# Optimization experiments

Hardware: AMD Instinct MI355X
Metric: run time of the kernel (lower is better)

Reference implementation:

```python
import jax, jax.numpy as jnp
import numpy as np

B, N, NB, E, H, A, K, D = 32, 512, 10, 1024, 256, 82, 4, 3


def setup_inputs() -> dict:
    key = jax.random.key(0)
    ks = iter(jax.random.split(key, 64))
    f = lambda shape: jax.random.normal(next(ks), shape, jnp.float32) * 0.05
    inp = {
        "atom_fea": jax.random.normal(next(ks), (B, N, A), jnp.float32),
        "bond_fea": jax.random.normal(next(ks), (B, E, 6), jnp.float32),
        "d_anb": jax.random.randint(next(ks), (B, N, NB), 0, N),
        "d_bnb": jax.random.randint(next(ks), (B, N, NB), 0, E),
        "d_nbs_mask": (jax.random.uniform(next(ks), (B, N, NB)) < 0.8).astype(jnp.float32),
        "d_mask": (jax.random.uniform(next(ks), (B, N)) < 0.9).astype(jnp.float32),
        "Wv": f((A, H)), "bv": f((H,)),
        "Wa_main": f((D, K, H, H)), "ba_main": f((D, K, H)),
        "Wa_super": f((D, K, H, H)), "ba_super": f((D, K, H)),
        "Wm": f((D, K, H, H)), "bm": f((D, K, H)),
        "Wbmm": f((D, K, H)), "bbmm": f((D, K)),
        "Wm2s": f((D, K * H, H)), "bm2s": f((D, H)),
        "Ws2m": f((D, H, H)), "bs2m": f((D, H)),
        "Wsup": f((D, H, H)), "bsup": f((D, H)),
        "Wzm1": f((D, H, H)), "bzm1": f((D, H)),
        "Wzm2": f((D, H, H)), "bzm2": f((D, H)),
        "Wzs1": f((D, H, H)), "bzs1": f((D, H)),
        "Wzs2": f((D, H, H)), "bzs2": f((D, H)),
        "Wu2": f((D, H + 6, H)), "bu2": f((D, H)),
        "Wu1": f((D, 2 * H, H)), "bu1": f((D, H)),
    }
    return inp


def mask_softmax(a, mask):
    a_max = jnp.max(a, -1, keepdims=True)
    e = jnp.exp(a - a_max) * mask
    return e / (jnp.sum(e, -1, keepdims=True) + 1e-6)


def _forward(atom_fea, bond_fea, d_nbs_mask, d_mask,
             Wv, bv, Wa_main, ba_main, Wa_super, ba_super, Wm, bm, Wbmm, bbmm,
             Wm2s, bm2s, Ws2m, bs2m, Wsup, bsup,
             Wzm1, bzm1, Wzm2, bzm2, Wzs1, bzs1, Wzs2, bzs2,
             Wu2, bu2, Wu1, bu1, d_anb, d_bnb):
    Bn = atom_fea.shape[0]
    bidx = jnp.arange(Bn)[:, None, None]
    # vertex embedding (default leaky_relu slope 0.01)
    vf = jax.nn.leaky_relu(atom_fea @ Wv + bv, 0.01)            # [B,N,H]
    sf = jnp.sum(vf * d_mask[:, :, None], axis=1, keepdims=True)  # [B,1,H]
    mask3 = d_nbs_mask[..., None]                               # [B,N,NB,1]
    for d in range(D):
        # --- multi-head main->super attention (vectorized over heads k) ---
        a_main = jnp.tanh(jnp.einsum('bnh,khj->bknj', vf, Wa_main[d]) + ba_main[d][None, :, None, :])
        a_super = jnp.tanh(jnp.einsum('boh,khj->bkoj', sf, Wa_super[d]) + ba_super[d][None, :, None, :])
        a = jnp.einsum('bknh,kh->bkn', a_main * a_super, Wbmm[d]) + bbmm[d][None, :, None]
        attn = mask_softmax(a, d_mask[:, None, :])               # [B,K,N]
        mvf = jnp.einsum('bnh,khj->bknj', vf, Wm[d]) + bm[d][None, :, None, :]
        m2s = jnp.einsum('bkn,bknh->bkh', attn, mvf).reshape(Bn, 1, K * H)
        main_to_super = jnp.tanh(m2s @ Wm2s[d] + bm2s[d])        # [B,1,H]
        # --- wln unit: gather neighbors, MLP, masked sum (slope 0.1) ---
        vnei = vf[bidx, d_anb]                                   # [B,N,NB,H]
        enei = bond_fea[bidx, d_bnb]                             # [B,N,NB,6]
        lnei = jnp.concatenate([vnei, enei], -1)                 # [B,N,NB,H+6]
        nei = jax.nn.leaky_relu(lnei @ Wu2[d] + bu2[d], 0.1)
        nei = jnp.sum(nei * mask3, axis=2)                       # [B,N,H]
        main_self = jax.nn.leaky_relu(jnp.concatenate([vf, nei], -1) @ Wu1[d] + bu1[d], 0.1)
        # --- GRU-style gated updates ---
        super_to_main = jnp.tanh(sf @ Ws2m[d] + bs2m[d])         # [B,1,H]
        super_self = jnp.tanh(sf @ Wsup[d] + bsup[d])            # [B,1,H]
        z_main = jax.nn.sigmoid(main_self @ Wzm1[d] + bzm1[d] + super_to_main @ Wzm2[d] + bzm2[d])
        vf = (1 - z_main) * main_self + z_main * super_to_main
        z_sup = jax.nn.sigmoid(super_self @ Wzs1[d] + bzs1[d] + main_to_super @ Wzs2[d] + bzs2[d])
        sf = (1 - z_sup) * super_self + z_sup * main_to_super    # [B,1,H]; sum over dim 1 is a no-op
    return vf, sf


def reference(atom_fea, bond_fea, d_anb, d_bnb, d_nbs_mask, d_mask,
              Wv, bv, Wa_main, ba_main, Wa_super, ba_super, Wm, bm, Wbmm, bbmm,
              Wm2s, bm2s, Ws2m, bs2m, Wsup, bsup,
              Wzm1, bzm1, Wzm2, bzm2, Wzs1, bzs1, Wzs2, bzs2,
              Wu2, bu2, Wu1, bu1):
    return _forward(atom_fea, bond_fea, d_nbs_mask, d_mask,
                    Wv, bv, Wa_main, ba_main, Wa_super, ba_super, Wm, bm, Wbmm, bbmm,
                    Wm2s, bm2s, Ws2m, bs2m, Wsup, bsup,
                    Wzm1, bzm1, Wzm2, bzm2, Wzs1, bzs1, Wzs2, bzs2,
                    Wu2, bu2, Wu1, bu1, d_anb, d_bnb)
```

## Files before the change

kernel.cpp:

```cpp
#include <hip/hip_runtime.h>
#include <hip/hip_bf16.h>

#define B_ 32
#define N_ 512
#define NB_ 10
#define E_ 1024
#define H_ 256
#define A_ 82
#define K_ 4
#define D_ 3
#define M_ (B_*N_)

typedef unsigned short u16;
typedef __attribute__((ext_vector_type(8))) short bf16x8;
typedef __attribute__((ext_vector_type(4))) float f32x4;

__device__ __forceinline__ float b2f(u16 u){
    unsigned int x = ((unsigned int)u) << 16;
    return __builtin_bit_cast(float, x);
}
__device__ __forceinline__ u16 f2b(float f){
    unsigned int x = __builtin_bit_cast(unsigned int, f);
    unsigned int lsb = (x >> 16) & 1u;
    x += 0x7fffu + lsb;
    return (u16)(x >> 16);
}
__device__ __forceinline__ float sigmoidf_(float x){ return 1.f/(1.f+expf(-x)); }

static constexpr int CVT_N[31] = {
    B_*E_*6, B_*N_*NB_, B_*N_,
    A_*H_, H_,
    D_*K_*H_*H_, D_*K_*H_, D_*K_*H_*H_, D_*K_*H_,
    D_*K_*H_*H_, D_*K_*H_, D_*K_*H_, D_*K_,
    D_*K_*H_*H_, D_*H_, D_*H_*H_, D_*H_,
    D_*H_*H_, D_*H_, D_*H_*H_, D_*H_,
    D_*H_*H_, D_*H_, D_*H_*H_, D_*H_,
    D_*H_*H_, D_*H_, D_*(H_+6)*H_, D_*H_,
    D_*2*H_*H_, D_*H_
};
struct Offs { long v[32]; };
static constexpr Offs mk_offs(){
    Offs o{}; o.v[0]=0;
    for(int i=0;i<31;i++) o.v[i+1]=o.v[i]+CVT_N[i];
    return o;
}
static constexpr Offs CVT_OFF = mk_offs();

struct Ptrs { const void* p[31]; };

__global__ void k_detect(const unsigned short* __restrict__ wv_raw, int* __restrict__ flag){
    float v = b2f(wv_raw[threadIdx.x]);
    bool plaus = (v==v) && (fabsf(v) < 100.0f);
    unsigned long long m = __ballot(plaus);
    if (threadIdx.x==0) *flag = (m == ~0ULL) ? 1 : 0;
}

__global__ void k_cvt(Ptrs ptrs, float* __restrict__ dst, const int* __restrict__ flag){
    int t = blockIdx.y;
    int n = CVT_N[t];
    int i4 = blockIdx.x*256 + threadIdx.x;
    if (i4*4 >= n) return;
    const void* src = ptrs.p[t];
    float4 o;
    if (*flag){
        ushort4 u = ((const ushort4*)src)[i4];
        o.x=b2f(u.x); o.y=b2f(u.y); o.z=b2f(u.z); o.w=b2f(u.w);
    } else {
        o = ((const float4*)src)[i4];
    }
    *(float4*)(dst + CVT_OFF.v[t] + (size_t)i4*4) = o;
}

__global__ void k_wt(const float* __restrict__ Wam, const float* __restrict__ Wu2,
                     const float* __restrict__ Wu1, const float* __restrict__ Wzm1,
                     u16* __restrict__ WT){
    int mi = blockIdx.z;
    const float* src;
    if (mi<12)      src = Wam  + (size_t)mi*H_*H_;
    else if (mi<15) src = Wu2  + (size_t)(mi-12)*(H_+6)*H_;
    else if (mi<18) src = Wu1  + (size_t)(mi-15)*2*H_*H_;
    else if (mi<21) src = Wu1  + (size_t)(mi-18)*2*H_*H_ + (size_t)H_*H_;
    else            src = Wzm1 + (size_t)(mi-21)*H_*H_;
    __shared__ float t[32][33];
    int x = threadIdx.x, y = threadIdx.y;
    int k0 = blockIdx.y*32, n0 = blockIdx.x*32;
    for(int yy=y; yy<32; yy+=8) t[yy][x] = src[(size_t)(k0+yy)*H_ + n0+x];
    __syncthreads();
    u16* dst = WT + ((size_t)mi*8 + (k0>>5))*8192;
    int quad = x>>3, j = x&7;
    for(int yy=y; yy<32; yy+=8){
        int n = n0+yy, nt = n>>4, lv = n&15;
        dst[nt*512 + quad*128 + lv*8 + j] = f2b(t[x][yy]);
    }
}

__global__ void k_embed(const u16* __restrict__ atom, const float* __restrict__ Wv,
                        const float* __restrict__ bv, float* __restrict__ vf,
                        u16* __restrict__ vf_bf, const int* __restrict__ flag){
    __shared__ float arow[8][A_];
    int r0 = blockIdx.x*8; int j = threadIdx.x;
    int fl = *flag;
    for(int i=j;i<8*A_;i+=256){
        int r=i/A_, a=i-r*A_;
        arow[r][a] = fl ? b2f(atom[(size_t)(r0+r)*A_+a])
                        : ((const float*)atom)[(size_t)(r0+r)*A_+a];
    }
    __syncthreads();
    float acc[8];
    float bj = bv[j];
    #pragma unroll
    for(int r=0;r<8;r++) acc[r]=bj;
    for(int a=0;a<A_;a++){
        float w = Wv[a*H_+j];
        #pragma unroll
        for(int r=0;r<8;r++) acc[r] += arow[r][a]*w;
    }
    #pragma unroll
    for(int r=0;r<8;r++){
        float v = acc[r];
        v = v>0.f ? v : 0.01f*v;
        vf[(size_t)(r0+r)*H_+j] = v;
        vf_bf[(size_t)(r0+r)*H_+j] = f2b(v);
    }
}

__global__ void k_sf0(const float* __restrict__ vf, const float* __restrict__ dmask,
                      float* __restrict__ sf){
    int b = blockIdx.x, h = threadIdx.x;
    __shared__ float mk[N_];
    for(int n=threadIdx.x;n<N_;n+=256) mk[n] = dmask[b*N_+n];
    __syncthreads();
    float s=0.f;
    #pragma unroll 8
    for(int n=0;n<N_;n++) s += mk[n]*vf[((size_t)b*N_+n)*H_ + h];
    sf[b*H_+h]=s;
}

__global__ void k_s1(int d, const float* __restrict__ sf,
    const float* __restrict__ Was, const float* __restrict__ bas,
    const float* __restrict__ Wbmm,
    const float* __restrict__ Ws2m, const float* __restrict__ bs2m,
    const float* __restrict__ Wsup, const float* __restrict__ bsup,
    float* __restrict__ asw, float* __restrict__ s2m, float* __restrict__ ssf)
{
    int b = blockIdx.x, m = blockIdx.y, j = threadIdx.x;
    __shared__ float sfl[H_];
    sfl[j] = sf[b*H_+j];
    __syncthreads();
    const float* W; float bias;
    if (m < 4){ W = Was + (size_t)(d*K_+m)*H_*H_; bias = bas[(d*K_+m)*H_+j]; }
    else if (m==4){ W = Ws2m + (size_t)d*H_*H_; bias = bs2m[d*H_+j]; }
    else { W = Wsup + (size_t)d*H_*H_; bias = bsup[d*H_+j]; }
    float acc = bias;
    #pragma unroll 8
    for(int h=0;h<H_;h++) acc += sfl[h]*W[h*H_+j];
    float v = tanhf(acc);
    if (m < 4) asw[(b*K_+m)*H_+j] = v * Wbmm[(d*K_+m)*H_+j];
    else if (m==4) s2m[b*H_+j] = v;
    else ssf[b*H_+j] = v;
}

__global__ void k_s2(int d, const float* __restrict__ s2m,
    const float* __restrict__ Wzm2, const float* __restrict__ bzm2,
    float* __restrict__ stm2p)
{
    int b=blockIdx.x, c=blockIdx.y, j=threadIdx.x;
    __shared__ float xl[64];
    if (j<64) xl[j] = s2m[b*H_ + c*64 + j];
    __syncthreads();
    const float* W = Wzm2 + (size_t)d*H_*H_ + (size_t)(c*64)*H_;
    float acc = (c==0) ? bzm2[d*H_+j] : 0.f;
    #pragma unroll 8
    for(int h=0;h<64;h++) acc += xl[h]*W[h*H_+j];
    stm2p[((size_t)c*B_+b)*H_+j] = acc;
}

__device__ __forceinline__ void stageW(const u16* __restrict__ g, u16* l){
    int t = threadIdx.x;
    const u16* gs = g + t*8;
    u16* ls = l + t*8;
    #pragma unroll
    for(int it=0; it<4; ++it)
        __builtin_amdgcn_global_load_lds(
            (const __attribute__((address_space(1))) void*)(gs + it*2048),
            (__attribute__((address_space(3))) void*)(ls + it*2048),
            16, 0, 0);
}

__device__ __forceinline__ void gemm_ldsW(const u16* __restrict__ Abf,
                                          const u16* __restrict__ WTg,
                                          u16* Wlds, f32x4 acc[2][8])
{
    int tid = threadIdx.x;
    int lane = tid & 63, wave = tid >> 6;
    int wy = wave >> 1, wx = wave & 1;
    int quad = lane >> 4, l15 = lane & 15;
    const u16* aP0 = Abf + (size_t)(wy*32 + l15)*H_ + quad*8;
    const u16* aP1 = aP0 + 16*H_;
    bf16x8 a[4][2];
    #pragma unroll
    for(int s=0;s<3;s++){
        a[s][0] = *(const bf16x8*)(aP0 + s*32);
        a[s][1] = *(const bf16x8*)(aP1 + s*32);
    }
    stageW(WTg, Wlds);
    #pragma unroll
    for(int mt=0;mt<2;mt++)
        #pragma unroll
        for(int nt=0;nt<8;nt++) acc[mt][nt]=(f32x4){0.f,0.f,0.f,0.f};
    __syncthreads();
    #pragma unroll
    for(int s=0;s<8;s++){
        if (s<7) stageW(WTg + (size_t)(s+1)*8192, Wlds + ((s+1)&1)*8192);
        if (s<5){
            int sl = s+3;
            a[sl&3][0] = *(const bf16x8*)(aP0 + sl*32);
            a[sl&3][1] = *(const bf16x8*)(aP1 + sl*32);
        }
        const u16* wb = Wlds + (s&1)*8192 + wx*4096 + quad*128 + l15*8;
        bf16x8 w[8];
        #pragma unroll
        for(int nt=0;nt<8;nt++) w[nt] = *(const bf16x8*)(wb + nt*512);
        #pragma unroll
        for(int mt=0;mt<2;mt++)
            #pragma unroll
            for(int nt=0;nt<8;nt++)
                acc[mt][nt] = __builtin_amdgcn_mfma_f32_16x16x32_bf16(
                    a[s&3][mt], w[nt], acc[mt][nt], 0,0,0);
        __syncthreads();
    }
}

__global__ __launch_bounds__(256,3) void k_gemm_big(int d, const u16* __restrict__ vf_bf,
    const u16* __restrict__ WT, const float* __restrict__ ba_main,
    const float* __restrict__ bbmm, const float* __restrict__ bu1,
    const float* __restrict__ asw, float* __restrict__ score,
    float* __restrict__ proj_u2, float* __restrict__ pu1a)
{
    __shared__ __attribute__((aligned(16))) u16 Wlds[2*8192];
    int m0 = blockIdx.x*64;
    int seg = blockIdx.y;
    int b = m0 >> 9;
    int mi;
    if (seg < 4)      mi = d*4+seg;
    else if (seg==4)  mi = 12+d;
    else              mi = 15+d;
    f32x4 acc[2][8];
    gemm_ldsW(vf_bf + (size_t)m0*H_, WT + (size_t)mi*H_*H_, Wlds, acc);
    int tid=threadIdx.x, lane=tid&63, wave=tid>>6;
    int wy=wave>>1, wx=wave&1, quad=lane>>4, l15=lane&15;
    if (seg < 4){
        float* sred = (float*)Wlds;
        const float* aswp = asw + (size_t)(b*K_+seg)*H_;
        const float* bap  = ba_main + (size_t)(d*K_+seg)*H_;
        float bbv[8], awv[8];
        #pragma unroll
        for(int nt=0;nt<8;nt++){
            int col = wx*128+nt*16+l15;
            bbv[nt]=bap[col]; awv[nt]=aswp[col];
        }
        #pragma unroll
        for(int mt=0;mt<2;mt++)
            #pragma unroll
            for(int r=0;r<4;r++){
                float p=0.f;
                #pragma unroll
                for(int nt=0;nt<8;nt++)
                    p += tanhf(acc[mt][nt][r]+bbv[nt])*awv[nt];
                int row = wy*32+mt*16+quad*4+r;
                sred[row*33 + wx*16+l15] = p;
            }
        __syncthreads();
        if (tid < 64){
            float s=0.f;
            #pragma unroll 8
            for(int i=0;i<32;i++) s += sred[tid*33+i];
            score[(size_t)(b*K_+seg)*N_ + (m0&511) + tid] = s + bbmm[d*K_+seg];
        }
    } else if (seg==4){
        #pragma unroll
        for(int mt=0;mt<2;mt++)
            #pragma unroll
            for(int nt=0;nt<8;nt++){
                int col = wx*128+nt*16+l15;
                #pragma unroll
                for(int r=0;r<4;r++){
                    int row = m0 + wy*32+mt*16+quad*4+r;
                    proj_u2[(size_t)row*H_+col] = acc[mt][nt][r];
                }
            }
    } else {
        const float* bp = bu1 + d*H_;
        #pragma unroll
        for(int mt=0;mt<2;mt++)
            #pragma unroll
            for(int nt=0;nt<8;nt++){
                int col = wx*128+nt*16+l15;
                float bb = bp[col];
                #pragma unroll
                for(int r=0;r<4;r++){
                    int row = m0 + wy*32+mt*16+quad*4+r;
                    pu1a[(size_t)row*H_+col] = acc[mt][nt][r] + bb;
                }
            }
    }
}

__global__ __launch_bounds__(256,3) void k_mainself(int d, u16* __restrict__ neims,
    const u16* __restrict__ WT, float* __restrict__ pu)
{
    __shared__ __attribute__((aligned(16))) u16 Wlds[2*8192];
    int m0 = blockIdx.x*64;
    f32x4 acc[2][8];
    gemm_ldsW(neims + (size_t)m0*H_, WT + (size_t)(18+d)*H_*H_, Wlds, acc);
    int tid=threadIdx.x, lane=tid&63, wave=tid>>6;
    int wy=wave>>1, wx=wave&1, quad=lane>>4, l15=lane&15;
    #pragma unroll
    for(int mt=0;mt<2;mt++)
        #pragma unroll
        for(int nt=0;nt<8;nt++){
            int col = wx*128+nt*16+l15;
            #pragma unroll
            for(int r=0;r<4;r++){
                int row = m0 + wy*32+mt*16+quad*4+r;
                float v = acc[mt][nt][r] + pu[(size_t)row*H_+col];
                v = v>0.f? v : 0.1f*v;
                pu[(size_t)row*H_+col] = v;
                neims[(size_t)row*H_+col] = f2b(v);
            }
        }
}

__global__ __launch_bounds__(256,3) void k_update(int d, const float* __restrict__ ms,
    const u16* __restrict__ ms_bf, const u16* __restrict__ WT, const float* __restrict__ bzm1,
    const float* __restrict__ stm2p, const float* __restrict__ s2m,
    float* __restrict__ vf, u16* __restrict__ vf_bf)
{
    __shared__ __attribute__((aligned(16))) u16 Wlds[2*8192];
    int m0 = blockIdx.x*64; int b = m0>>9;
    f32x4 acc[2][8];
    gemm_ldsW(ms_bf + (size_t)m0*H_, WT + (size_t)(21+d)*H_*H_, Wlds, acc);
    int tid=threadIdx.x, lane=tid&63, wave=tid>>6;
    int wy=wave>>1, wx=wave&1, quad=lane>>4, l15=lane&15;
    #pragma unroll
    for(int mt=0;mt<2;mt++)
        #pragma unroll
        for(int nt=0;nt<8;nt++){
            int col = wx*128+nt*16+l15;
            float bz = bzm1[d*H_+col];
            float st = stm2p[(size_t)(0*B_+b)*H_+col] + stm2p[(size_t)(1*B_+b)*H_+col]
                     + stm2p[(size_t)(2*B_+b)*H_+col] + stm2p[(size_t)(3*B_+b)*H_+col];
            float sm = s2m[b*H_+col];
            #pragma unroll
            for(int r=0;r<4;r++){
                int row = m0 + wy*32+mt*16+quad*4+r;
                float z = sigmoidf_(acc[mt][nt][r] + bz + st);
                float msv = ms[(size_t)row*H_+col];
                float o = (1.f-z)*msv + z*sm;
                vf[(size_t)row*H_+col] = o;
                vf_bf[(size_t)row*H_+col] = f2b(o);
            }
        }
}

__global__ void k_softmax(float* __restrict__ score, const float* __restrict__ dmask,
                          float* __restrict__ sumattn){
    int b = blockIdx.x, k = blockIdx.y;
    int tid = threadIdx.x;
    __shared__ float sh[256];
    float* a = score + (size_t)(b*K_+k)*N_;
    float v0 = a[tid], v1 = a[tid+256];
    sh[tid]=fmaxf(v0,v1); __syncthreads();
    for(int s=128;s>0;s>>=1){ if(tid<s) sh[tid]=fmaxf(sh[tid],sh[tid+s]); __syncthreads(); }
    float m = sh[0]; __syncthreads();
    float e0 = expf(v0-m)*dmask[b*N_+tid], e1 = expf(v1-m)*dmask[b*N_+tid+256];
    sh[tid]=e0+e1; __syncthreads();
    for(int s=128;s>0;s>>=1){ if(tid<s) sh[tid]+=sh[tid+s]; __syncthreads(); }
    float S = sh[0];
    float inv = 1.f/(S+1e-6f);
    a[tid]=e0*inv; a[tid+256]=e1*inv;
    if(tid==0) sumattn[b*K_+k]=S*inv;
}

__global__ void k_t2(const float* __restrict__ attn, const float* __restrict__ vf,
                     float* __restrict__ tpart){
    int b=blockIdx.x, k=blockIdx.y, c=blockIdx.z, h=threadIdx.x;
    __shared__ float at[256];
    at[h] = attn[(size_t)(b*K_+k)*N_ + c*256 + h];
    __syncthreads();
    float acc=0.f;
    const float* vfp = vf + ((size_t)b*N_ + c*256)*H_ + h;
    #pragma unroll 8
    for(int n=0;n<256;n++) acc += at[n]*vfp[(size_t)n*H_];
    tpart[((size_t)(c*B_+b)*K_+k)*H_+h]=acc;
}

__global__ void k_m1(int d, const float* __restrict__ tpart, const float* __restrict__ sumattn,
    const float* __restrict__ Wm, const float* __restrict__ bm, float* __restrict__ m2s)
{
    int b=blockIdx.x, k=blockIdx.y, j=threadIdx.x;
    __shared__ float tl[H_];
    tl[j] = tpart[((size_t)(0*B_+b)*K_+k)*H_+j] + tpart[((size_t)(1*B_+b)*K_+k)*H_+j];
    __syncthreads();
    const float* W = Wm + (size_t)(d*K_+k)*H_*H_;
    float acc = sumattn[b*K_+k]*bm[(d*K_+k)*H_+j];
    #pragma unroll 8
    for(int h=0;h<H_;h++) acc += tl[h]*W[h*H_+j];
    m2s[(size_t)(b*K_+k)*H_+j]=acc;
}

__global__ void k_m2(int d, const float* __restrict__ m2s, const float* __restrict__ Wm2s,
                     float* __restrict__ mtsp)
{
    int b=blockIdx.x, c=blockIdx.y, j=threadIdx.x;
    __shared__ float xl[H_];
    xl[j]=m2s[(size_t)(b*K_+c)*H_+j];
    __syncthreads();
    const float* W = Wm2s + (size_t)d*(K_*H_)*H_ + (size_t)(c*H_)*H_;
    float acc=0.f;
    #pragma unroll 8
    for(int h=0;h<H_;h++) acc += xl[h]*W[h*H_+j];
    mtsp[((size_t)c*B_+b)*H_+j]=acc;
}

__global__ void k_mts(int d, const float* __restrict__ mtsp, const float* __restrict__ bm2s,
                      float* __restrict__ mts){
    int b=blockIdx.x, j=threadIdx.x;
    float acc = bm2s[d*H_+j];
    #pragma unroll
    for(int c=0;c<4;c++) acc += mtsp[((size_t)c*B_+b)*H_+j];
    mts[b*H_+j]=tanhf(acc);
}

__global__ void k_m3(int d, const float* __restrict__ ssf, const float* __restrict__ mts,
    const float* __restrict__ Wzs1, const float* __restrict__ Wzs2,
    float* __restrict__ p1, float* __restrict__ p2)
{
    int b=blockIdx.x, m=blockIdx.y, j=threadIdx.x;
    __shared__ float xl[H_];
    const float* x = m ? mts : ssf;
    xl[j]=x[b*H_+j];
    __syncthreads();
    const float* W = (m ? Wzs2 : Wzs1) + (size_t)d*H_*H_;
    float acc=0.f;
    #pragma unroll 8
    for(int h=0;h<H_;h++) acc += xl[h]*W[h*H_+j];
    (m ? p2 : p1)[b*H_+j]=acc;
}

__global__ void k_sfup(int d, const float* __restrict__ p1, const float* __restrict__ p2,
    const float* __restrict__ bzs1, const float* __restrict__ bzs2,
    const float* __restrict__ ssf, const float* __restrict__ mts, float* __restrict__ sf)
{
    int b=blockIdx.x, j=threadIdx.x;
    float z = sigmoidf_(p1[b*H_+j]+bzs1[d*H_+j]+p2[b*H_+j]+bzs2[d*H_+j]);
    sf[b*H_+j]=(1.f-z)*ssf[b*H_+j]+z*mts[b*H_+j];
}

__global__ void k_nei(int d, const int* __restrict__ anb, const int* __restrict__ bnb,
    const float* __restrict__ nbm, const float* __restrict__ bond,
    const float* __restrict__ Wu2, const float* __restrict__ bu2,
    const float* __restrict__ proj_u2, u16* __restrict__ nei_bf)
{
    __shared__ float W2s[6][256];
    __shared__ float bfeat[4][NB_][6];
    __shared__ int ai[4][NB_]; __shared__ int bi[4][NB_]; __shared__ float mk[4][NB_];
    int r0 = blockIdx.x*4; int b = r0 >> 9; int h = threadIdx.x;
    const float* W2 = Wu2 + (size_t)d*(H_+6)*H_ + (size_t)H_*H_;
    for(int i=h;i<6*H_;i+=256) W2s[i>>8][i&255] = W2[i];
    if (h < 4*NB_){
        int r=h/NB_, jn=h-r*NB_;
        ai[r][jn]=anb[(size_t)(r0+r)*NB_+jn];
        bi[r][jn]=bnb[(size_t)(r0+r)*NB_+jn];
        mk[r][jn]=nbm[(size_t)(r0+r)*NB_+jn];
    }
    __syncthreads();
    if (h < 4*NB_*6){
        int r=h/(NB_*6), rem=h-r*(NB_*6), jn=rem/6, i=rem-jn*6;
        bfeat[r][jn][i]=bond[((size_t)b*E_+bi[r][jn])*6+i];
    }
    __syncthreads();
    float bu = bu2[d*H_+h];
    #pragma unroll
    for(int r=0;r<4;r++){
        float acc=0.f;
        #pragma unroll
        for(int jn=0;jn<NB_;jn++){
            float v = proj_u2[((size_t)b*N_+ai[r][jn])*H_+h] + bu;
            #pragma unroll
            for(int i=0;i<6;i++) v += bfeat[r][jn][i]*W2s[i][h];
            v = v>0.f? v : 0.1f*v;
            acc += mk[r][jn]*v;
        }
        nei_bf[(size_t)(r0+r)*H_+h]=f2b(acc);
    }
}

__global__ void k_out(const float* __restrict__ vf, const float* __restrict__ sf,
                      void* __restrict__ out, const int* __restrict__ flag){
    int idx = blockIdx.x*256 + threadIdx.x;
    const int total = M_*H_ + B_*H_;
    if (idx >= total) return;
    float v = (idx < M_*H_) ? vf[idx] : sf[idx - M_*H_];
    if (*flag) ((unsigned short*)out)[idx] = f2b(v);
    else       ((float*)out)[idx] = v;
}

extern "C" void kernel_launch(void* const* d_in, const int* in_sizes, int n_in,
                              void* d_out, int out_size, void* d_ws, size_t ws_size,
                              hipStream_t stream)
{
    const int* anb = (const int*)d_in[2];
    const int* bnb = (const int*)d_in[3];

    float* ws   = (float*)d_ws;
    int*   flag = (int*)ws;
    float* cvt  = ws + 64;
    float* p    = cvt + ((CVT_OFF.v[31] + 63) & ~63L);
    float* vf        = p; p += (size_t)M_*H_;
    float* proj_u2   = p; p += (size_t)M_*H_;
    float* proj_u1a  = p; p += (size_t)M_*H_;
    u16*   vf_bf     = (u16*)p; p += (size_t)M_*H_/2;
    u16*   neims     = (u16*)p; p += (size_t)M_*H_/2;
    float* sf        = p; p += B_*H_;
    float* score     = p; p += B_*K_*N_;
    float* sumattn   = p; p += B_*K_;
    float* asw       = p; p += B_*K_*H_;
    float* s2m       = p; p += B_*H_;
    float* ssf       = p; p += B_*H_;
    float* stm2p     = p; p += 4*B_*H_;
    float* tpart     = p; p += 2*B_*K_*H_;
    float* m2s       = p; p += B_*K_*H_;
    float* mtsp      = p; p += 4*B_*H_;
    float* mts       = p; p += B_*H_;
    float* p1        = p; p += B_*H_;
    float* p2        = p; p += B_*H_;
    u16*   WT        = (u16*)p;

    const float* cBond = cvt + CVT_OFF.v[0];
    const float* cNbm  = cvt + CVT_OFF.v[1];
    const float* cDm   = cvt + CVT_OFF.v[2];
    const float* cWv   = cvt + CVT_OFF.v[3];
    const float* cbv   = cvt + CVT_OFF.v[4];
    const float* cWam  = cvt + CVT_OFF.v[5];
    const float* cbam  = cvt + CVT_OFF.v[6];
    const float* cWas  = cvt + CVT_OFF.v[7];
    const float* cbas  = cvt + CVT_OFF.v[8];
    const float* cWm   = cvt + CVT_OFF.v[9];
    const float* cbm   = cvt + CVT_OFF.v[10];
    const float* cWbmm = cvt + CVT_OFF.v[11];
    const float* cbbmm = cvt + CVT_OFF.v[12];
    const float* cWm2s = cvt + CVT_OFF.v[13];
    const float* cbm2s = cvt + CVT_OFF.v[14];
    const float* cWs2m = cvt + CVT_OFF.v[15];
    const float* cbs2m = cvt + CVT_OFF.v[16];
    const float* cWsup = cvt + CVT_OFF.v[17];
    const float* cbsup = cvt + CVT_OFF.v[18];
    const float* cWzm1 = cvt + CVT_OFF.v[19];
    const float* cbzm1 = cvt + CVT_OFF.v[20];
    const float* cWzm2 = cvt + CVT_OFF.v[21];
    const float* cbzm2 = cvt + CVT_OFF.v[22];
    const float* cWzs1 = cvt + CVT_OFF.v[23];
    const float* cbzs1 = cvt + CVT_OFF.v[24];
    const float* cWzs2 = cvt + CVT_OFF.v[25];
    const float* cbzs2 = cvt + CVT_OFF.v[26];
    const float* cWu2  = cvt + CVT_OFF.v[27];
    const float* cbu2  = cvt + CVT_OFF.v[28];
    const float* cWu1  = cvt + CVT_OFF.v[29];
    const float* cbu1  = cvt + CVT_OFF.v[30];

    Ptrs ptrs;
    {
        int idx[31] = {1,4,5,6,7,8,9,10,11,12,13,14,15,16,17,18,19,20,21,
                       22,23,24,25,26,27,28,29,30,31,32,33};
        for(int i=0;i<31;i++) ptrs.p[i] = d_in[idx[i]];
    }

    k_detect<<<1,64,0,stream>>>((const unsigned short*)d_in[6], flag);
    {
        int maxv4 = (D_*K_*H_*H_ + 3)/4;
        int gx = (maxv4 + 255)/256;
        k_cvt<<<dim3(gx,31),256,0,stream>>>(ptrs, cvt, flag);
    }
    k_wt<<<dim3(8,8,24),dim3(32,8),0,stream>>>(cWam, cWu2, cWu1, cWzm1, WT);

    k_embed<<<M_/8,256,0,stream>>>((const u16*)d_in[0], cWv, cbv, vf, vf_bf, flag);
    k_sf0<<<B_,256,0,stream>>>(vf, cDm, sf);
    for(int d=0; d<D_; d++){
        k_s1<<<dim3(B_,6),256,0,stream>>>(d, sf, cWas, cbas, cWbmm,
                                          cWs2m, cbs2m, cWsup, cbsup, asw, s2m, ssf);
        k_s2<<<dim3(B_,4),256,0,stream>>>(d, s2m, cWzm2, cbzm2, stm2p);
        k_gemm_big<<<dim3(M_/64,6),256,0,stream>>>(d, vf_bf, WT, cbam, cbbmm, cbu1,
                                                   asw, score, proj_u2, proj_u1a);
        k_softmax<<<dim3(B_,K_),256,0,stream>>>(score, cDm, sumattn);
        k_t2<<<dim3(B_,K_,2),256,0,stream>>>(score, vf, tpart);
        k_m1<<<dim3(B_,K_),256,0,stream>>>(d, tpart, sumattn, cWm, cbm, m2s);
        k_m2<<<dim3(B_,4),256,0,stream>>>(d, m2s, cWm2s, mtsp);
        k_mts<<<B_,256,0,stream>>>(d, mtsp, cbm2s, mts);
        k_m3<<<dim3(B_,2),256,0,stream>>>(d, ssf, mts, cWzs1, cWzs2, p1, p2);
        k_sfup<<<B_,256,0,stream>>>(d, p1, p2, cbzs1, cbzs2, ssf, mts, sf);
        k_nei<<<M_/4,256,0,stream>>>(d, anb, bnb, cNbm, cBond, cWu2, cbu2, proj_u2, neims);
        k_mainself<<<M_/64,256,0,stream>>>(d, neims, WT, proj_u1a);
        k_update<<<M_/64,256,0,stream>>>(d, proj_u1a, neims, WT, cbzm1, stm2p, s2m, vf, vf_bf);
    }
    k_out<<<(M_*H_+B_*H_+255)/256,256,0,stream>>>(vf, sf, d_out, flag);
}
```

Baseline: 725.4 us.

## Fuse per-depth kernel chain: merge mainself+update, softmax+attn, super-node tail kernels

```diff
diff --git a/kernel.cpp b/kernel.cpp
--- a/kernel.cpp
+++ b/kernel.cpp
@@ -56,19 +56,23 @@
 }
 
 __global__ void k_cvt(Ptrs ptrs, float* __restrict__ dst, const int* __restrict__ flag){
-    int t = blockIdx.y;
-    int n = CVT_N[t];
-    int i4 = blockIdx.x*256 + threadIdx.x;
-    if (i4*4 >= n) return;
+    long i4 = (long)blockIdx.x*256 + threadIdx.x;
+    const long TOT4 = CVT_OFF.v[31]/4;
+    if (i4 >= TOT4) return;
+    long e = i4*4;
+    int t = 0;
+    #pragma unroll
+    for(int i=1;i<31;i++) t += (e >= CVT_OFF.v[i]) ? 1 : 0;
+    long l4 = i4 - CVT_OFF.v[t]/4;
     const void* src = ptrs.p[t];
     float4 o;
     if (*flag){
-        ushort4 u = ((const ushort4*)src)[i4];
+        ushort4 u = ((const ushort4*)src)[l4];
         o.x=b2f(u.x); o.y=b2f(u.y); o.z=b2f(u.z); o.w=b2f(u.w);
     } else {
-        o = ((const float4*)src)[i4];
-    }
-    *(float4*)(dst + CVT_OFF.v[t] + (size_t)i4*4) = o;
+        o = ((const float4*)src)[l4];
+    }
+    *(float4*)(dst + CVT_OFF.v[t] + l4*4) = o;
 }
 
 __global__ void k_wt(const float* __restrict__ Wam, const float* __restrict__ Wu2,
@@ -141,12 +145,29 @@
     const float* __restrict__ Wbmm,
     const float* __restrict__ Ws2m, const float* __restrict__ bs2m,
     const float* __restrict__ Wsup, const float* __restrict__ bsup,
-    float* __restrict__ asw, float* __restrict__ s2m, float* __restrict__ ssf)
+    const float* __restrict__ Wzm2, const float* __restrict__ bzm2,
+    float* __restrict__ asw, float* __restrict__ s2m, float* __restrict__ ssf,
+    float* __restrict__ st)
 {
     int b = blockIdx.x, m = blockIdx.y, j = threadIdx.x;
     __shared__ float sfl[H_];
+    __shared__ float s2l[H_];
     sfl[j] = sf[b*H_+j];
     __syncthreads();
+    if (m == 6){
+        const float* W = Ws2m + (size_t)d*H_*H_;
+        float acc = bs2m[d*H_+j];
+        #pragma unroll 8
+        for(int h=0;h<H_;h++) acc += sfl[h]*W[h*H_+j];
+        s2l[j] = tanhf(acc);
+        __syncthreads();
+        const float* W2 = Wzm2 + (size_t)d*H_*H_;
+        float acc2 = bzm2[d*H_+j];
+        #pragma unroll 8
+        for(int h=0;h<H_;h++) acc2 += s2l[h]*W2[h*H_+j];
+        st[b*H_+j] = acc2;
+        return;
+    }
     const float* W; float bias;
     if (m < 4){ W = Was + (size_t)(d*K_+m)*H_*H_; bias = bas[(d*K_+m)*H_+j]; }
     else if (m==4){ W = Ws2m + (size_t)d*H_*H_; bias = bs2m[d*H_+j]; }
@@ -160,21 +181,6 @@
     else ssf[b*H_+j] = v;
 }
 
-__global__ void k_s2(int d, const float* __restrict__ s2m,
-    const float* __restrict__ Wzm2, const float* __restrict__ bzm2,
-    float* __restrict__ stm2p)
-{
-    int b=blockIdx.x, c=blockIdx.y, j=threadIdx.x;
-    __shared__ float xl[64];
-    if (j<64) xl[j] = s2m[b*H_ + c*64 + j];
-    __syncthreads();
-    const float* W = Wzm2 + (size_t)d*H_*H_ + (size_t)(c*64)*H_;
-    float acc = (c==0) ? bzm2[d*H_+j] : 0.f;
-    #pragma unroll 8
-    for(int h=0;h<64;h++) acc += xl[h]*W[h*H_+j];
-    stm2p[((size_t)c*B_+b)*H_+j] = acc;
-}
-
 __device__ __forceinline__ void stageW(const u16* __restrict__ g, u16* l){
     int t = threadIdx.x;
     const u16* gs = g + t*8;
@@ -227,6 +233,39 @@
             for(int nt=0;nt<8;nt++)
                 acc[mt][nt] = __builtin_amdgcn_mfma_f32_16x16x32_bf16(
                     a[s&3][mt], w[nt], acc[mt][nt], 0,0,0);
+        __syncthreads();
+    }
+}
+
+__device__ __forceinline__ void gemm_lds2(const u16* Als, const u16* __restrict__ WTg,
+                                          u16* Wlds, f32x4 acc[2][8])
+{
+    int tid = threadIdx.x;
+    int lane = tid & 63, wave = tid >> 6;
+    int wy = wave >> 1, wx = wave & 1;
+    int quad = lane >> 4, l15 = lane & 15;
+    stageW(WTg, Wlds);
+    #pragma unroll
+    for(int mt=0;mt<2;mt++)
+        #pragma unroll
+        for(int nt=0;nt<8;nt++) acc[mt][nt]=(f32x4){0.f,0.f,0.f,0.f};
+    __syncthreads();
+    int r0 = wy*32 + l15, r1 = r0 + 16;
+    #pragma unroll
+    for(int s=0;s<8;s++){
+        if (s<7) stageW(WTg + (size_t)(s+1)*8192, Wlds + ((s+1)&1)*8192);
+        int c0 = s*32 + quad*8;
+        bf16x8 a0 = *(const bf16x8*)(Als + r0*256 + (c0 ^ ((r0&7)<<3)));
+        bf16x8 a1 = *(const bf16x8*)(Als + r1*256 + (c0 ^ ((r1&7)<<3)));
+        const u16* wb = Wlds + (s&1)*8192 + wx*4096 + quad*128 + l15*8;
+        bf16x8 w[8];
+        #pragma unroll
+        for(int nt=0;nt<8;nt++) w[nt] = *(const bf16x8*)(wb + nt*512);
+        #pragma unroll
+        for(int nt=0;nt<8;nt++){
+            acc[0][nt] = __builtin_amdgcn_mfma_f32_16x16x32_bf16(a0, w[nt], acc[0][nt], 0,0,0);
+            acc[1][nt] = __builtin_amdgcn_mfma_f32_16x16x32_bf16(a1, w[nt], acc[1][nt], 0,0,0);
+        }
         __syncthreads();
     }
 }
@@ -306,11 +345,14 @@
     }
 }
 
-__global__ __launch_bounds__(256,3) void k_mainself(int d, u16* __restrict__ neims,
-    const u16* __restrict__ WT, float* __restrict__ pu)
+__global__ __launch_bounds__(256,2) void k_msup(int d, const u16* __restrict__ neims,
+    const u16* __restrict__ WT, const float* __restrict__ pu1a,
+    const float* __restrict__ bzm1, const float* __restrict__ st,
+    const float* __restrict__ s2m, float* __restrict__ vf, u16* __restrict__ vf_bf)
 {
     __shared__ __attribute__((aligned(16))) u16 Wlds[2*8192];
-    int m0 = blockIdx.x*64;
+    __shared__ __attribute__((aligned(16))) u16 ms_lds[64*256];
+    int m0 = blockIdx.x*64; int b = m0>>9;
     f32x4 acc[2][8];
     gemm_ldsW(neims + (size_t)m0*H_, WT + (size_t)(18+d)*H_*H_, Wlds, acc);
     int tid=threadIdx.x, lane=tid&63, wave=tid>>6;
@@ -322,40 +364,28 @@
             int col = wx*128+nt*16+l15;
             #pragma unroll
             for(int r=0;r<4;r++){
-                int row = m0 + wy*32+mt*16+quad*4+r;
-                float v = acc[mt][nt][r] + pu[(size_t)row*H_+col];
+                int rl = wy*32+mt*16+quad*4+r;
+                float v = acc[mt][nt][r] + pu1a[(size_t)(m0+rl)*H_+col];
                 v = v>0.f? v : 0.1f*v;
-                pu[(size_t)row*H_+col] = v;
-                neims[(size_t)row*H_+col] = f2b(v);
+                acc[mt][nt][r] = v;
+                ms_lds[rl*256 + (col ^ ((rl&7)<<3))] = f2b(v);
             }
         }
-}
-
-__global__ __launch_bounds__(256,3) void k_update(int d, const float* __restrict__ ms,
-    const u16* __restrict__ ms_bf, const u16* __restrict__ WT, const float* __restrict__ bzm1,
-    const float* __restrict__ stm2p, const float* __restrict__ s2m,
-    float* __restrict__ vf, u16* __restrict__ vf_bf)
-{
-    __shared__ __attribute__((aligned(16))) u16 Wlds[2*8192];
-    int m0 = blockIdx.x*64; int b = m0>>9;
-    f32x4 acc[2][8];
-    gemm_ldsW(ms_bf + (size_t)m0*H_, WT + (size_t)(21+d)*H_*H_, Wlds, acc);
-    int tid=threadIdx.x, lane=tid&63, wave=tid>>6;
-    int wy=wave>>1, wx=wave&1, quad=lane>>4, l15=lane&15;
+    f32x4 acc2[2][8];
+    gemm_lds2(ms_lds, WT + (size_t)(21+d)*H_*H_, Wlds, acc2);
     #pragma unroll
     for(int mt=0;mt<2;mt++)
         #pragma unroll
         for(int nt=0;nt<8;nt++){
             int col = wx*128+nt*16+l15;
             float bz = bzm1[d*H_+col];
-            float st = stm2p[(size_t)(0*B_+b)*H_+col] + stm2p[(size_t)(1*B_+b)*H_+col]
-                     + stm2p[(size_t)(2*B_+b)*H_+col] + stm2p[(size_t)(3*B_+b)*H_+col];
+            float stv = st[b*H_+col];
             float sm = s2m[b*H_+col];
             #pragma unroll
             for(int r=0;r<4;r++){
                 int row = m0 + wy*32+mt*16+quad*4+r;
-                float z = sigmoidf_(acc[mt][nt][r] + bz + st);
-                float msv = ms[(size_t)row*H_+col];
+                float z = sigmoidf_(acc2[mt][nt][r] + bz + stv);
+                float msv = acc[mt][nt][r];
                 float o = (1.f-z)*msv + z*sm;
                 vf[(size_t)row*H_+col] = o;
                 vf_bf[(size_t)row*H_+col] = f2b(o);
@@ -363,50 +393,53 @@
         }
 }
 
-__global__ void k_softmax(float* __restrict__ score, const float* __restrict__ dmask,
-                          float* __restrict__ sumattn){
-    int b = blockIdx.x, k = blockIdx.y;
-    int tid = threadIdx.x;
+__global__ __launch_bounds__(512) void k_att(int d, const float* __restrict__ score,
+    const float* __restrict__ dmask, const float* __restrict__ vf,
+    const float* __restrict__ Wm, const float* __restrict__ bm,
+    float* __restrict__ m2s)
+{
+    int b = blockIdx.x, k = blockIdx.y, tid = threadIdx.x;
+    __shared__ float at[N_];
     __shared__ float sh[256];
-    float* a = score + (size_t)(b*K_+k)*N_;
-    float v0 = a[tid], v1 = a[tid+256];
-    sh[tid]=fmaxf(v0,v1); __syncthreads();
+    __shared__ float tp[2][256];
+    const float* a = score + (size_t)(b*K_+k)*N_;
+    float v0=0.f, v1=0.f, e0=0.f, e1=0.f;
+    if (tid < 256){ v0=a[tid]; v1=a[tid+256]; sh[tid]=fmaxf(v0,v1); }
+    __syncthreads();
     for(int s=128;s>0;s>>=1){ if(tid<s) sh[tid]=fmaxf(sh[tid],sh[tid+s]); __syncthreads(); }
     float m = sh[0]; __syncthreads();
-    float e0 = expf(v0-m)*dmask[b*N_+tid], e1 = expf(v1-m)*dmask[b*N_+tid+256];
-    sh[tid]=e0+e1; __syncthreads();
+    if (tid < 256){
+        e0 = expf(v0-m)*dmask[b*N_+tid];
+        e1 = expf(v1-m)*dmask[b*N_+tid+256];
+        sh[tid]=e0+e1;
+    }
+    __syncthreads();
     for(int s=128;s>0;s>>=1){ if(tid<s) sh[tid]+=sh[tid+s]; __syncthreads(); }
     float S = sh[0];
     float inv = 1.f/(S+1e-6f);
-    a[tid]=e0*inv; a[tid+256]=e1*inv;
-    if(tid==0) sumattn[b*K_+k]=S*inv;
-}
-
-__global__ void k_t2(const float* __restrict__ attn, const float* __restrict__ vf,
-                     float* __restrict__ tpart){
-    int b=blockIdx.x, k=blockIdx.y, c=blockIdx.z, h=threadIdx.x;
-    __shared__ float at[256];
-    at[h] = attn[(size_t)(b*K_+k)*N_ + c*256 + h];
-    __syncthreads();
-    float acc=0.f;
-    const float* vfp = vf + ((size_t)b*N_ + c*256)*H_ + h;
-    #pragma unroll 8
-    for(int n=0;n<256;n++) acc += at[n]*vfp[(size_t)n*H_];
-    tpart[((size_t)(c*B_+b)*K_+k)*H_+h]=acc;
-}
-
-__global__ void k_m1(int d, const float* __restrict__ tpart, const float* __restrict__ sumattn,
-    const float* __restrict__ Wm, const float* __restrict__ bm, float* __restrict__ m2s)
-{
-    int b=blockIdx.x, k=blockIdx.y, j=threadIdx.x;
-    __shared__ float tl[H_];
-    tl[j] = tpart[((size_t)(0*B_+b)*K_+k)*H_+j] + tpart[((size_t)(1*B_+b)*K_+k)*H_+j];
-    __syncthreads();
-    const float* W = Wm + (size_t)(d*K_+k)*H_*H_;
-    float acc = sumattn[b*K_+k]*bm[(d*K_+k)*H_+j];
-    #pragma unroll 8
-    for(int h=0;h<H_;h++) acc += tl[h]*W[h*H_+j];
-    m2s[(size_t)(b*K_+k)*H_+j]=acc;
+    float sumattn = S*inv;
+    if (tid < 256){ at[tid]=e0*inv; at[tid+256]=e1*inv; }
+    __syncthreads();
+    int h = tid & 255, half = tid >> 8;
+    {
+        float acc=0.f;
+        const float* vfp = vf + ((size_t)b*N_ + half*256)*H_ + h;
+        const float* atp = at + half*256;
+        #pragma unroll 8
+        for(int n=0;n<256;n++) acc += atp[n]*vfp[(size_t)n*H_];
+        tp[half][h]=acc;
+    }
+    __syncthreads();
+    {
+        const float* W = Wm + (size_t)(d*K_+k)*H_*H_;
+        float acc = (half==0) ? sumattn*bm[(d*K_+k)*H_+h] : 0.f;
+        int h0 = half*128;
+        #pragma unroll 8
+        for(int t2=h0; t2<h0+128; t2++) acc += (tp[0][t2]+tp[1][t2])*W[(size_t)t2*H_+h];
+        at[half*256+h]=acc;
+    }
+    __syncthreads();
+    if (tid < 256) m2s[(size_t)(b*K_+k)*H_+tid] = at[tid]+at[256+tid];
 }
 
 __global__ void k_m2(int d, const float* __restrict__ m2s, const float* __restrict__ Wm2s,
@@ -423,38 +456,37 @@
     mtsp[((size_t)c*B_+b)*H_+j]=acc;
 }
 
-__global__ void k_mts(int d, const float* __restrict__ mtsp, const float* __restrict__ bm2s,
-                      float* __restrict__ mts){
-    int b=blockIdx.x, j=threadIdx.x;
-    float acc = bm2s[d*H_+j];
-    #pragma unroll
-    for(int c=0;c<4;c++) acc += mtsp[((size_t)c*B_+b)*H_+j];
-    mts[b*H_+j]=tanhf(acc);
-}
-
-__global__ void k_m3(int d, const float* __restrict__ ssf, const float* __restrict__ mts,
+__global__ __launch_bounds__(512) void k_fin(int d, const float* __restrict__ mtsp,
+    const float* __restrict__ bm2s, const float* __restrict__ ssf,
     const float* __restrict__ Wzs1, const float* __restrict__ Wzs2,
-    float* __restrict__ p1, float* __restrict__ p2)
-{
-    int b=blockIdx.x, m=blockIdx.y, j=threadIdx.x;
-    __shared__ float xl[H_];
-    const float* x = m ? mts : ssf;
-    xl[j]=x[b*H_+j];
-    __syncthreads();
-    const float* W = (m ? Wzs2 : Wzs1) + (size_t)d*H_*H_;
-    float acc=0.f;
-    #pragma unroll 8
-    for(int h=0;h<H_;h++) acc += xl[h]*W[h*H_+j];
-    (m ? p2 : p1)[b*H_+j]=acc;
-}
-
-__global__ void k_sfup(int d, const float* __restrict__ p1, const float* __restrict__ p2,
     const float* __restrict__ bzs1, const float* __restrict__ bzs2,
-    const float* __restrict__ ssf, const float* __restrict__ mts, float* __restrict__ sf)
-{
-    int b=blockIdx.x, j=threadIdx.x;
-    float z = sigmoidf_(p1[b*H_+j]+bzs1[d*H_+j]+p2[b*H_+j]+bzs2[d*H_+j]);
-    sf[b*H_+j]=(1.f-z)*ssf[b*H_+j]+z*mts[b*H_+j];
+    float* __restrict__ sf)
+{
+    int b = blockIdx.x, tid = threadIdx.x;
+    int j = tid & 255, g = tid >> 8;
+    __shared__ float mtsl[256], ssl[256], pp[2][256];
+    if (g==0){
+        float acc = bm2s[d*H_+j];
+        #pragma unroll
+        for(int c=0;c<4;c++) acc += mtsp[((size_t)c*B_+b)*H_+j];
+        mtsl[j] = tanhf(acc);
+    } else {
+        ssl[j] = ssf[b*H_+j];
+    }
+    __syncthreads();
+    {
+        const float* W = (g ? Wzs2 : Wzs1) + (size_t)d*H_*H_;
+        const float* x = g ? mtsl : ssl;
+        float acc = 0.f;
+        #pragma unroll 8
+        for(int h=0;h<H_;h++) acc += x[h]*W[h*H_+j];
+        pp[g][j] = acc;
+    }
+    __syncthreads();
+    if (g==0){
+        float z = sigmoidf_(pp[0][j]+bzs1[d*H_+j]+pp[1][j]+bzs2[d*H_+j]);
+        sf[b*H_+j] = (1.f-z)*ssl[j] + z*mtsl[j];
+    }
 }
 
 __global__ void k_nei(int d, const int* __restrict__ anb, const int* __restrict__ bnb,
@@ -524,17 +556,12 @@
     u16*   neims     = (u16*)p; p += (size_t)M_*H_/2;
     float* sf        = p; p += B_*H_;
     float* score     = p; p += B_*K_*N_;
-    float* sumattn   = p; p += B_*K_;
     float* asw       = p; p += B_*K_*H_;
     float* s2m       = p; p += B_*H_;
     float* ssf       = p; p += B_*H_;
-    float* stm2p     = p; p += 4*B_*H_;
-    float* tpart     = p; p += 2*B_*K_*H_;
+    float* st        = p; p += B_*H_;
     float* m2s       = p; p += B_*K_*H_;
     float* mtsp      = p; p += 4*B_*H_;
-    float* mts       = p; p += B_*H_;
-    float* p1        = p; p += B_*H_;
-    float* p2        = p; p += B_*H_;
     u16*   WT        = (u16*)p;
 
     const float* cBond = cvt + CVT_OFF.v[0];
@@ -578,30 +605,25 @@
 
     k_detect<<<1,64,0,stream>>>((const unsigned short*)d_in[6], flag);
     {
-        int maxv4 = (D_*K_*H_*H_ + 3)/4;
-        int gx = (maxv4 + 255)/256;
-        k_cvt<<<dim3(gx,31),256,0,stream>>>(ptrs, cvt, flag);
+        long tot4 = CVT_OFF.v[31]/4;
+        int gx = (int)((tot4 + 255)/256);
+        k_cvt<<<gx,256,0,stream>>>(ptrs, cvt, flag);
     }
     k_wt<<<dim3(8,8,24),dim3(32,8),0,stream>>>(cWam, cWu2, cWu1, cWzm1, WT);
 
     k_embed<<<M_/8,256,0,stream>>>((const u16*)d_in[0], cWv, cbv, vf, vf_bf, flag);
     k_sf0<<<B_,256,0,stream>>>(vf, cDm, sf);
     for(int d=0; d<D_; d++){
-        k_s1<<<dim3(B_,6),256,0,stream>>>(d, sf, cWas, cbas, cWbmm,
-                                          cWs2m, cbs2m, cWsup, cbsup, asw, s2m, ssf);
-        k_s2<<<dim3(B_,4),256,0,stream>>>(d, s2m, cWzm2, cbzm2, stm2p);
+        k_s1<<<dim3(B_,7),256,0,stream>>>(d, sf, cWas, cbas, cWbmm,
+                                          cWs2m, cbs2m, cWsup, cbsup,
+                                          cWzm2, cbzm2, asw, s2m, ssf, st);
         k_gemm_big<<<dim3(M_/64,6),256,0,stream>>>(d, vf_bf, WT, cbam, cbbmm, cbu1,
                                                    asw, score, proj_u2, proj_u1a);
-        k_softmax<<<dim3(B_,K_),256,0,stream>>>(score, cDm, sumattn);
-        k_t2<<<dim3(B_,K_,2),256,0,stream>>>(score, vf, tpart);
-        k_m1<<<dim3(B_,K_),256,0,stream>>>(d, tpart, sumattn, cWm, cbm, m2s);
+        k_att<<<dim3(B_,K_),512,0,stream>>>(d, score, cDm, vf, cWm, cbm, m2s);
+        k_nei<<<M_/4,256,0,stream>>>(d, anb, bnb, cNbm, cBond, cWu2, cbu2, proj_u2, neims);
+        k_msup<<<M_/64,256,0,stream>>>(d, neims, WT, proj_u1a, cbzm1, st, s2m, vf, vf_bf);
         k_m2<<<dim3(B_,4),256,0,stream>>>(d, m2s, cWm2s, mtsp);
-        k_mts<<<B_,256,0,stream>>>(d, mtsp, cbm2s, mts);
-        k_m3<<<dim3(B_,2),256,0,stream>>>(d, ssf, mts, cWzs1, cWzs2, p1, p2);
-        k_sfup<<<B_,256,0,stream>>>(d, p1, p2, cbzs1, cbzs2, ssf, mts, sf);
-        k_nei<<<M_/4,256,0,stream>>>(d, anb, bnb, cNbm, cBond, cWu2, cbu2, proj_u2, neims);
-        k_mainself<<<M_/64,256,0,stream>>>(d, neims, WT, proj_u1a);
-        k_update<<<M_/64,256,0,stream>>>(d, proj_u1a, neims, WT, cbzm1, stm2p, s2m, vf, vf_bf);
+        k_fin<<<B_,512,0,stream>>>(d, mtsp, cbm2s, ssf, cWzs1, cWzs2, cbzs1, cbzs2, sf);
     }
     k_out<<<(M_*H_+B_*H_+255)/256,256,0,stream>>>(vf, sf, d_out, flag);
 }
```

Measured after the change: 651.6 us. 1.11x faster.
